# Kernel optimization log

Measured on AMD Instinct MI355X. Metric: run time of the kernel, lower is better.

Reference implementation:

```python
import jax, jax.numpy as jnp
import numpy as np

K = 20  # number of nearest neighbors (includes self, distance 0, as in torch topk(largest=False))


def edge_feature(x, k):
    """x: (B, C, N) -> edge features (B, N, k, 2C) = concat[central, neighbor - central]."""
    sq = jnp.sum(x * x, axis=1)                       # (B, N)
    inner = jnp.einsum('bcn,bcm->bnm', x, x)          # (B, N, N)
    d = sq[:, :, None] + sq[:, None, :] - 2.0 * inner # squared pairwise distance
    _, idx = jax.lax.top_k(-d, k)                     # (B, N, k) nearest indices (incl. self)
    xT = jnp.transpose(x, (0, 2, 1))                  # (B, N, C)
    # nb[b,n,j,c] = xT[b, idx[b,n,j], c]
    nb = jnp.take_along_axis(xT[:, :, None, :], idx[:, :, :, None], axis=1)  # (B, N, k, C)
    central = jnp.broadcast_to(xT[:, :, None, :], nb.shape)
    return jnp.concatenate([central, nb - central], axis=-1)  # (B, N, k, 2C)


def setup_inputs() -> dict:
    key = jax.random.key(0)
    ks = jax.random.split(key, 13)
    B, C, N = 8, 3, 4096
    def w(k_, shape, fan_in):
        return (jax.random.normal(k_, shape, dtype=jnp.float32) / np.sqrt(fan_in)).astype(jnp.float32)
    inp = {
        'x':  jax.random.normal(ks[0], (B, C, N), dtype=jnp.float32),
        # local 1x1 conv2d weights (out_ch, in_ch)
        'W1': w(ks[1], (64, 6), 6),        'b1': jnp.zeros((64,), jnp.float32),
        'W2': w(ks[2], (128, 64), 64),     'b2': jnp.zeros((128,), jnp.float32),
        # inter 1x1 conv1d
        'W3': w(ks[3], (1024, 128), 128),  'b3': jnp.zeros((1024,), jnp.float32),
        # global FC
        'W4': w(ks[4], (512, 1024), 1024), 'b4': jnp.zeros((512,), jnp.float32),
        'W5': w(ks[5], (256, 512), 512),   'b5': jnp.zeros((256,), jnp.float32),
        # final linear (torch inits this to zeros -> identity output; use small random for a
        # non-trivial correctness baseline, same math path)
        'W6': 0.01 * w(ks[6], (9, 256), 256), 'b6': jnp.zeros((9,), jnp.float32),
    }
    return inp


def reference(x, W1, b1, W2, b2, W3, b3, W4, b4, W5, b5, W6, b6):
    e = edge_feature(x, K)                                     # (B, N, k, 6)
    h = jax.nn.relu(jnp.einsum('bnkc,oc->bnko', e, W1) + b1)   # (B, N, k, 64)
    h = jax.nn.relu(jnp.einsum('bnkc,oc->bnko', h, W2) + b2)   # (B, N, k, 128)
    h = jnp.max(h, axis=2)                                     # max over k -> (B, N, 128)
    h = jax.nn.relu(jnp.einsum('bnc,oc->bno', h, W3) + b3)     # (B, N, 1024)
    g = jnp.max(h, axis=1)                                     # max over points -> (B, 1024)
    g = jax.nn.relu(g @ W4.T + b4)                             # (B, 512)
    g = jax.nn.relu(g @ W5.T + b5)                             # (B, 256)
    t = g @ W6.T + b6                                          # (B, 9)
    Bsz = x.shape[0]
    out_ch, in_ch = 3, 3
    t = t.reshape(Bsz, out_ch, in_ch) + jnp.eye(out_ch, in_ch, dtype=t.dtype)
    return t
```

## Files before the change

kernel.cpp:

```cpp
#include <hip/hip_runtime.h>
#include <hip/hip_bf16.h>
#include <cstdint>

#define B_SZ 8
#define NPTS 4096
#define KNN  20
#define NTOT (B_SZ * NPTS)
#define PPB  8
#define NPREP 1093

typedef unsigned int uint;
typedef unsigned short ushort;
using short8 = __attribute__((ext_vector_type(8))) short;
using f32x4  = __attribute__((ext_vector_type(4))) float;

__device__ __forceinline__ ushort f2bf(float f) {
  uint u = __float_as_uint(f);
  u += 0x7fff + ((u >> 16) & 1);
  return (ushort)(u >> 16);
}
__device__ __forceinline__ float bf2f(ushort h) {
  return __uint_as_float(((uint)h) << 16);
}
__device__ __forceinline__ uint fenc(float f) {
  uint u = __float_as_uint(f);
  return (u & 0x80000000u) ? ~u : (u | 0x80000000u);
}
__device__ __forceinline__ float fdec(uint e) {
  uint u = (e & 0x80000000u) ? (e & 0x7fffffffu) : ~e;
  return __uint_as_float(u);
}

__device__ __forceinline__ void sortf64(float& v, int lane) {
  #pragma unroll
  for (int k = 2; k <= 64; k <<= 1) {
    #pragma unroll
    for (int j = k >> 1; j > 0; j >>= 1) {
      float o = __shfl_xor(v, j, 64);
      bool keepmin = (((lane & k) == 0) == ((lane & j) == 0));
      bool lt = v < o;
      v = (keepmin == lt) ? v : o;
    }
  }
}

__device__ __forceinline__ void sortu64(unsigned long long& v, int lane) {
  #pragma unroll
  for (int k = 2; k <= 64; k <<= 1) {
    #pragma unroll
    for (int j = k >> 1; j > 0; j >>= 1) {
      unsigned long long o = __shfl_xor(v, j, 64);
      bool keepmin = (((lane & k) == 0) == ((lane & j) == 0));
      bool lt = v < o;
      v = (keepmin == lt) ? v : o;
    }
  }
}

__global__ void knn_prep_kernel(
    const float* __restrict__ x,  const float* __restrict__ W1,
    const float* __restrict__ W3, const float* __restrict__ W2,
    ushort* __restrict__ u, ushort* __restrict__ W3b, ushort* __restrict__ W2b,
    uint* __restrict__ g_enc, int* __restrict__ idx_out) {
  __shared__ int surv[4][256];
  __shared__ int cnt[4];

  if (blockIdx.x < NPREP) {
    int blk = blockIdx.x;
    if (blk < 1024) {
      int t = blk * 256 + threadIdx.x;
      int p = t >> 3, c0 = (t & 7) * 8;
      int b = p >> 12, n = p & (NPTS - 1);
      const float* xb = x + (size_t)b * 3 * NPTS;
      float x0 = xb[n], x1 = xb[NPTS + n], x2 = xb[2 * NPTS + n];
      uint pk[4];
      #pragma unroll
      for (int j = 0; j < 8; ++j) {
        const float* w = W1 + (c0 + j) * 6;
        float v = w[3] * x0 + w[4] * x1 + w[5] * x2;
        ushort h = f2bf(v);
        if (j & 1) pk[j >> 1] |= ((uint)h << 16); else pk[j >> 1] = h;
      }
      uint4 q; q.x = pk[0]; q.y = pk[1]; q.z = pk[2]; q.w = pk[3];
      *reinterpret_cast<uint4*>(u + (size_t)p * 64 + c0) = q;
    } else if (blk < 1088) {
      int t = (blk - 1024) * 256 + threadIdx.x;
      const float4* src = reinterpret_cast<const float4*>(W3 + t * 8);
      float4 f0 = src[0], f1 = src[1];
      uint4 pk;
      pk.x = (uint)f2bf(f0.x) | ((uint)f2bf(f0.y) << 16);
      pk.y = (uint)f2bf(f0.z) | ((uint)f2bf(f0.w) << 16);
      pk.z = (uint)f2bf(f1.x) | ((uint)f2bf(f1.y) << 16);
      pk.w = (uint)f2bf(f1.z) | ((uint)f2bf(f1.w) << 16);
      *reinterpret_cast<uint4*>(W3b + t * 8) = pk;
    } else if (blk < 1092) {
      int t = (blk - 1088) * 256 + threadIdx.x;
      const float4* src = reinterpret_cast<const float4*>(W2 + t * 8);
      float4 f0 = src[0], f1 = src[1];
      uint4 pk;
      pk.x = (uint)f2bf(f0.x) | ((uint)f2bf(f0.y) << 16);
      pk.y = (uint)f2bf(f0.z) | ((uint)f2bf(f0.w) << 16);
      pk.z = (uint)f2bf(f1.x) | ((uint)f2bf(f1.y) << 16);
      pk.w = (uint)f2bf(f1.z) | ((uint)f2bf(f1.w) << 16);
      *reinterpret_cast<uint4*>(W2b + t * 8) = pk;
    } else {
      for (int i = threadIdx.x; i < B_SZ * 1024; i += 256) g_enc[i] = 0;
    }
    return;
  }

  const unsigned long long INFK = ~0ull;
  int w = threadIdx.x >> 6, lane = threadIdx.x & 63;
  int row = (blockIdx.x - NPREP) * 4 + w;
  int b = row >> 12, n = row & (NPTS - 1);
  const float* xb = x + (size_t)b * 3 * NPTS;
  float qx = xb[n], qy = xb[NPTS + n], qz = xb[2 * NPTS + n];
  if (lane == 0) cnt[w] = 0;

  const float4* X0 = reinterpret_cast<const float4*>(xb);
  const float4* X1 = reinterpret_cast<const float4*>(xb + NPTS);
  const float4* X2 = reinterpret_cast<const float4*>(xb + 2 * NPTS);

  uint kreg[32];
  float bm = 3.0e38f;
  #pragma unroll
  for (int i = 0; i < 16; ++i) {
    int v4 = i * 64 + lane;
    float4 a0 = X0[v4], a1 = X1[v4], a2 = X2[v4];
    float dx, dy, dz, d0, d1, d2, d3;
    dx = a0.x - qx; dy = a1.x - qy; dz = a2.x - qz; d0 = dx*dx + dy*dy + dz*dz;
    dx = a0.y - qx; dy = a1.y - qy; dz = a2.y - qz; d1 = dx*dx + dy*dy + dz*dz;
    dx = a0.z - qx; dy = a1.z - qy; dz = a2.z - qz; d2 = dx*dx + dy*dy + dz*dz;
    dx = a0.w - qx; dy = a1.w - qy; dz = a2.w - qz; d3 = dx*dx + dy*dy + dz*dz;
    bm = fminf(bm, fminf(fminf(d0, d1), fminf(d2, d3)));
    kreg[2*i]   = (__float_as_uint(d0) >> 16) | (__float_as_uint(d1) & 0xFFFF0000u);
    kreg[2*i+1] = (__float_as_uint(d2) >> 16) | (__float_as_uint(d3) & 0xFFFF0000u);
  }

  sortf64(bm, lane);
  float T = __shfl(bm, 19, 64);
  uint T16 = __float_as_uint(T) >> 16;

  asm volatile("s_waitcnt lgkmcnt(0)" ::: "memory");
  #pragma unroll
  for (int i = 0; i < 16; ++i) {
    uint ka = kreg[2*i], kb = kreg[2*i+1];
    int m0 = (i * 64 + lane) * 4;
    if ((ka & 0xffffu) <= T16) { int s = atomicAdd(&cnt[w], 1); if (s < 256) surv[w][s] = m0; }
    if ((ka >> 16)     <= T16) { int s = atomicAdd(&cnt[w], 1); if (s < 256) surv[w][s] = m0 + 1; }
    if ((kb & 0xffffu) <= T16) { int s = atomicAdd(&cnt[w], 1); if (s < 256) surv[w][s] = m0 + 2; }
    if ((kb >> 16)     <= T16) { int s = atomicAdd(&cnt[w], 1); if (s < 256) surv[w][s] = m0 + 3; }
  }
  asm volatile("s_waitcnt lgkmcnt(0)" ::: "memory");
  int M = cnt[w];

  if (M <= 256) {
    unsigned long long run = INFK;
    int nch = (M + 63) >> 6;
    for (int c = 0; c < nch; ++c) {
      int s = c * 64 + lane;
      unsigned long long v = INFK;
      if (s < M) {
        int m = surv[w][s];
        float dx = xb[m] - qx, dy = xb[NPTS + m] - qy, dz = xb[2 * NPTS + m] - qz;
        float d = dx * dx + dy * dy + dz * dz;
        v = ((unsigned long long)__float_as_uint(d) << 32) | (unsigned)m;
      }
      sortu64(v, lane);
      if (c == 0) {
        run = v;
      } else {
        unsigned long long b19 = __shfl(v, (19 - lane) & 63, 64);
        unsigned long long cand = run < b19 ? run : b19;
        run = (lane < KNN) ? cand : INFK;
        sortu64(run, lane);
      }
    }
    if (lane < KNN) idx_out[(size_t)row * KNN + lane] = (int)(run & 0xFFFFFFFFull);
  } else {
    unsigned long long prev = 0ull;
    for (int r = 0; r < KNN; ++r) {
      unsigned long long best = INFK;
      for (int i = 0; i < 16; ++i) {
        int v4 = i * 64 + lane;
        float4 a0 = X0[v4], a1 = X1[v4], a2 = X2[v4];
        float dx, dy, dz, d[4];
        dx = a0.x - qx; dy = a1.x - qy; dz = a2.x - qz; d[0] = dx*dx + dy*dy + dz*dz;
        dx = a0.y - qx; dy = a1.y - qy; dz = a2.y - qz; d[1] = dx*dx + dy*dy + dz*dz;
        dx = a0.z - qx; dy = a1.z - qy; dz = a2.z - qz; d[2] = dx*dx + dy*dy + dz*dz;
        dx = a0.w - qx; dy = a1.w - qy; dz = a2.w - qz; d[3] = dx*dx + dy*dy + dz*dz;
        #pragma unroll
        for (int j = 0; j < 4; ++j) {
          int m = i * 256 + lane * 4 + j;
          unsigned long long key =
              ((unsigned long long)__float_as_uint(d[j]) << 32) | (unsigned)m;
          if ((r == 0 || key > prev) && key < best) best = key;
        }
      }
      #pragma unroll
      for (int off = 32; off; off >>= 1) {
        unsigned long long o = __shfl_xor(best, off, 64);
        best = o < best ? o : best;
      }
      if (lane == 0) idx_out[(size_t)row * KNN + r] = (int)(best & 0xFFFFFFFFull);
      prev = best;
    }
  }
}

__global__ __launch_bounds__(256, 4) void edge_kernel(
    const float* __restrict__ x,  const float* __restrict__ W1, const float* __restrict__ b1,
    const ushort* __restrict__ W2b, const float* __restrict__ b2,
    const ushort* __restrict__ u, const int* __restrict__ idx,
    ushort* __restrict__ h128b) {
  __shared__ __align__(16) char h1s[PPB * 32 * 128];
  __shared__ float vs[PPB * 64];
  __shared__ int   nbs[PPB * KNN];

  int tid = threadIdx.x, w = tid >> 6, l = tid & 63;
  int p0 = blockIdx.x * PPB;
  int b = p0 >> 12;
  const float* xb = x + (size_t)b * 3 * NPTS;

  for (int t = tid; t < PPB * 64; t += 256) {
    int p = t >> 6, c = t & 63;
    int n = (p0 + p) & (NPTS - 1);
    float x0 = xb[n], x1 = xb[NPTS + n], x2 = xb[2 * NPTS + n];
    const float* wr = W1 + c * 6;
    vs[t] = (wr[0] - wr[3]) * x0 + (wr[1] - wr[4]) * x1 + (wr[2] - wr[5]) * x2 + b1[c];
  }
  if (tid < PPB * KNN) nbs[tid] = idx[(size_t)p0 * KNN + tid];

  short8 bfr[8][2];
  #pragma unroll
  for (int nt = 0; nt < 8; ++nt) {
    #pragma unroll
    for (int ks = 0; ks < 2; ++ks) {
      bfr[nt][ks] = *(const short8*)(W2b + (nt * 16 + (l & 15)) * 64
                                         + ks * 32 + (l >> 4) * 8);
    }
  }
  __syncthreads();

  const ushort* ub = u + (((size_t)b) << 12) * 64;
  #pragma unroll
  for (int j = 0; j < 8; ++j) {
    int e_loc = j * 8 + (l >> 3);
    int p_loc = (w << 1) + (e_loc >> 5);
    int e_in = e_loc & 31;
    int e_src = (e_in < KNN) ? e_in : e_in - KNN;
    int nb = nbs[p_loc * KNN + e_src];
    int c0 = (l & 7) * 8;
    uint4 uv = *(const uint4*)(ub + (((size_t)nb) << 6) + c0);
    const float* vp = vs + p_loc * 64 + c0;
    float4 v0 = *(const float4*)vp, v1 = *(const float4*)(vp + 4);
    float h0 = fmaxf(bf2f((ushort)(uv.x & 0xffff)) + v0.x, 0.f);
    float h1 = fmaxf(bf2f((ushort)(uv.x >> 16))    + v0.y, 0.f);
    float h2 = fmaxf(bf2f((ushort)(uv.y & 0xffff)) + v0.z, 0.f);
    float h3 = fmaxf(bf2f((ushort)(uv.y >> 16))    + v0.w, 0.f);
    float h4 = fmaxf(bf2f((ushort)(uv.z & 0xffff)) + v1.x, 0.f);
    float h5 = fmaxf(bf2f((ushort)(uv.z >> 16))    + v1.y, 0.f);
    float h6 = fmaxf(bf2f((ushort)(uv.w & 0xffff)) + v1.z, 0.f);
    float h7 = fmaxf(bf2f((ushort)(uv.w >> 16))    + v1.w, 0.f);
    uint4 pk;
    pk.x = (uint)f2bf(h0) | ((uint)f2bf(h1) << 16);
    pk.y = (uint)f2bf(h2) | ((uint)f2bf(h3) << 16);
    pk.z = (uint)f2bf(h4) | ((uint)f2bf(h5) << 16);
    pk.w = (uint)f2bf(h6) | ((uint)f2bf(h7) << 16);
    int row = (w << 6) + e_loc;
    int byte = (row * 128 + c0 * 2) ^ ((row & 7) << 4);
    *(uint4*)(h1s + byte) = pk;
  }
  __syncthreads();

  float bias0 = b2[l], bias1 = b2[64 + l];

  #pragma unroll
  for (int pt = 0; pt < 2; ++pt) {
    int rbase = (w << 6) + (pt << 5);
    short8 a[2][2];
    #pragma unroll
    for (int m = 0; m < 2; ++m) {
      #pragma unroll
      for (int ks = 0; ks < 2; ++ks) {
        int row = rbase + m * 16 + (l & 15);
        int byte = (row * 128 + ks * 64 + (l >> 4) * 16) ^ ((row & 7) << 4);
        a[m][ks] = *(const short8*)(h1s + byte);
      }
    }
    float r03 = 0.f, r47 = 0.f;
    #pragma unroll
    for (int nt = 0; nt < 8; ++nt) {
      f32x4 acc0 = {0.f, 0.f, 0.f, 0.f}, acc1 = {0.f, 0.f, 0.f, 0.f};
      acc0 = __builtin_amdgcn_mfma_f32_16x16x32_bf16(a[0][0], bfr[nt][0], acc0, 0, 0, 0);
      acc0 = __builtin_amdgcn_mfma_f32_16x16x32_bf16(a[0][1], bfr[nt][1], acc0, 0, 0, 0);
      acc1 = __builtin_amdgcn_mfma_f32_16x16x32_bf16(a[1][0], bfr[nt][0], acc1, 0, 0, 0);
      acc1 = __builtin_amdgcn_mfma_f32_16x16x32_bf16(a[1][1], bfr[nt][1], acc1, 0, 0, 0);
      float m0 = fmaxf(fmaxf(fmaxf(acc0[0], acc1[0]), fmaxf(acc0[1], acc1[1])),
                       fmaxf(fmaxf(acc0[2], acc1[2]), fmaxf(acc0[3], acc1[3])));
      m0 = fmaxf(m0, __shfl_xor(m0, 16, 64));
      m0 = fmaxf(m0, __shfl_xor(m0, 32, 64));
      if ((l >> 4) == (nt & 3)) { if (nt < 4) r03 = m0; else r47 = m0; }
    }
    int pg = p0 + (w << 1) + pt;
    h128b[(size_t)pg * 128 + l]      = f2bf(fmaxf(r03 + bias0, 0.f));
    h128b[(size_t)pg * 128 + 64 + l] = f2bf(fmaxf(r47 + bias1, 0.f));
  }
}

__global__ __launch_bounds__(256, 2) void inter_kernel(
    const ushort* __restrict__ h128b, const ushort* __restrict__ W3b,
    uint* __restrict__ g_enc) {
  __shared__ __align__(16) char as_[64 * 256];
  int tid = threadIdx.x, w = tid >> 6, l = tid & 63;
  int chunk = blockIdx.x;
  const ushort* hp = h128b + (size_t)chunk * 64 * 128;

  {
    int row = tid >> 2, q = tid & 3;
    const uint4* src = reinterpret_cast<const uint4*>(hp + row * 128 + q * 32);
    int sw = (row & 7) << 4;
    int base = row * 256 + q * 64;
    #pragma unroll
    for (int k = 0; k < 4; ++k)
      *(uint4*)(as_ + ((base + k * 16) ^ sw)) = src[k];
  }
  __syncthreads();

  short8 a[4][4];
  #pragma unroll
  for (int m = 0; m < 4; ++m) {
    #pragma unroll
    for (int ks = 0; ks < 4; ++ks) {
      int row = m * 16 + (l & 15);
      int byte = (row * 256 + ks * 64 + (l >> 4) * 16) ^ ((row & 7) << 4);
      a[m][ks] = *(const short8*)(as_ + byte);
    }
  }

  const ushort* wb = W3b + (size_t)(w * 256) * 128;
  float res[4];
  #pragma unroll
  for (int nt = 0; nt < 16; ++nt) {
    f32x4 acc0 = {0.f,0.f,0.f,0.f}, acc1 = {0.f,0.f,0.f,0.f};
    f32x4 acc2 = {0.f,0.f,0.f,0.f}, acc3 = {0.f,0.f,0.f,0.f};
    #pragma unroll
    for (int ks = 0; ks < 4; ++ks) {
      short8 bf = *(const short8*)(wb + (size_t)(nt * 16 + (l & 15)) * 128
                                      + ks * 32 + (l >> 4) * 8);
      acc0 = __builtin_amdgcn_mfma_f32_16x16x32_bf16(a[0][ks], bf, acc0, 0, 0, 0);
      acc1 = __builtin_amdgcn_mfma_f32_16x16x32_bf16(a[1][ks], bf, acc1, 0, 0, 0);
      acc2 = __builtin_amdgcn_mfma_f32_16x16x32_bf16(a[2][ks], bf, acc2, 0, 0, 0);
      acc3 = __builtin_amdgcn_mfma_f32_16x16x32_bf16(a[3][ks], bf, acc3, 0, 0, 0);
    }
    float m01 = fmaxf(fmaxf(fmaxf(acc0[0], acc1[0]), fmaxf(acc0[1], acc1[1])),
                      fmaxf(fmaxf(acc0[2], acc1[2]), fmaxf(acc0[3], acc1[3])));
    float m23 = fmaxf(fmaxf(fmaxf(acc2[0], acc3[0]), fmaxf(acc2[1], acc3[1])),
                      fmaxf(fmaxf(acc2[2], acc3[2]), fmaxf(acc2[3], acc3[3])));
    float m0 = fmaxf(m01, m23);
    m0 = fmaxf(m0, __shfl_xor(m0, 16, 64));
    m0 = fmaxf(m0, __shfl_xor(m0, 32, 64));
    if ((l >> 4) == (nt & 3)) res[nt >> 2] = m0;
  }
  uint* ge = g_enc + (size_t)(chunk >> 6) * 1024 + w * 256;
  #pragma unroll
  for (int g = 0; g < 4; ++g) atomicMax(ge + g * 64 + l, fenc(res[g]));
}

__global__ __launch_bounds__(64) void fc_kernel(const float* __restrict__ in,
                                                const uint* __restrict__ enc,
                                                const float* __restrict__ pre_b,
                                                const float* __restrict__ W,
                                                const float* __restrict__ bias,
                                                float* __restrict__ out,
                                                int in_dim, int out_dim, int mode) {
  int blk = blockIdx.x;
  int b = blk / out_dim, o = blk % out_dim;
  int lane = threadIdx.x;
  const float* w = W + (size_t)o * in_dim;
  float s = 0.f;
  for (int c = lane; c < in_dim; c += 64) {
    float v;
    if (mode == 2) v = fmaxf(fdec(enc[(size_t)b * in_dim + c]) + pre_b[c], 0.f);
    else           v = in[(size_t)b * in_dim + c];
    s += v * w[c];
  }
  #pragma unroll
  for (int off = 32; off; off >>= 1) s += __shfl_down(s, off);
  if (lane == 0) {
    float r = s + bias[o];
    if (mode != 1) r = fmaxf(r, 0.0f);
    else if (o == 0 || o == 4 || o == 8) r += 1.0f;
    out[blk] = r;
  }
}

extern "C" void kernel_launch(void* const* d_in, const int* in_sizes, int n_in,
                              void* d_out, int out_size, void* d_ws, size_t ws_size,
                              hipStream_t stream) {
  const float* x  = (const float*)d_in[0];
  const float* W1 = (const float*)d_in[1];
  const float* b1 = (const float*)d_in[2];
  const float* W2 = (const float*)d_in[3];
  const float* b2 = (const float*)d_in[4];
  const float* W3 = (const float*)d_in[5];
  const float* b3 = (const float*)d_in[6];
  const float* W4 = (const float*)d_in[7];
  const float* b4 = (const float*)d_in[8];
  const float* W5 = (const float*)d_in[9];
  const float* b5 = (const float*)d_in[10];
  const float* W6 = (const float*)d_in[11];
  const float* b6 = (const float*)d_in[12];
  float* out = (float*)d_out;

  char* ws = (char*)d_ws;
  ushort* u_bf  = (ushort*)(ws);
  int*    idxb  = (int*)  (ws + (8u  << 20));
  ushort* h128b = (ushort*)(ws + (11u << 20));
  ushort* W3b   = (ushort*)(ws + (27u << 20));
  ushort* W2b   = (ushort*)(ws + (27u << 20) + (256u << 10));
  uint*   g_enc = (uint*) (ws + (5u  << 20));
  float*  g4    = (float*)(ws + (6u  << 20));
  float*  g5    = (float*)(ws + (7u  << 20));

  hipLaunchKernelGGL(knn_prep_kernel, dim3(NPREP + 8192), dim3(256), 0, stream,
                     x, W1, W3, W2, u_bf, W3b, W2b, g_enc, idxb);
  hipLaunchKernelGGL(edge_kernel, dim3(NTOT / PPB), dim3(256), 0, stream,
                     x, W1, b1, W2b, b2, u_bf, idxb, h128b);
  hipLaunchKernelGGL(inter_kernel, dim3(512), dim3(256), 0, stream, h128b, W3b, g_enc);
  hipLaunchKernelGGL(fc_kernel, dim3(B_SZ * 512), dim3(64), 0, stream,
                     nullptr, g_enc, b3, W4, b4, g4, 1024, 512, 2);
  hipLaunchKernelGGL(fc_kernel, dim3(B_SZ * 256), dim3(64), 0, stream,
                     g4, nullptr, nullptr, W5, b5, g5, 512, 256, 0);
  hipLaunchKernelGGL(fc_kernel, dim3(B_SZ * 9),   dim3(64), 0, stream,
                     g5, nullptr, nullptr, W6, b6, out, 256, 9, 1);
}
```

Before: 167.6 us.

## Process two KNN query rows per wavefront to share point loads and interleave sorts

Each wavefront now handles two query points instead of one. The float4 loads of the point cloud are shared between both distance computations, and the bitonic shuffle sorts are run on two values at once to expose instruction-level parallelism. The KNN portion of the grid is halved to match. This cuts redundant global/L2 loads and shuffle latency stalls, at the cost of roughly doubled register use (two 32-entry key arrays) and possibly lower occupancy.

```diff
diff --git a/kernel.cpp b/kernel.cpp
--- a/kernel.cpp
+++ b/kernel.cpp
@@ -31,28 +31,31 @@
   return __uint_as_float(u);
 }
 
-__device__ __forceinline__ void sortf64(float& v, int lane) {
+__device__ __forceinline__ void sortf64x2(float& v0, float& v1, int lane) {
   #pragma unroll
   for (int k = 2; k <= 64; k <<= 1) {
     #pragma unroll
     for (int j = k >> 1; j > 0; j >>= 1) {
-      float o = __shfl_xor(v, j, 64);
+      float o0 = __shfl_xor(v0, j, 64);
+      float o1 = __shfl_xor(v1, j, 64);
       bool keepmin = (((lane & k) == 0) == ((lane & j) == 0));
-      bool lt = v < o;
-      v = (keepmin == lt) ? v : o;
-    }
-  }
-}
-
-__device__ __forceinline__ void sortu64(unsigned long long& v, int lane) {
+      bool lt0 = v0 < o0; v0 = (keepmin == lt0) ? v0 : o0;
+      bool lt1 = v1 < o1; v1 = (keepmin == lt1) ? v1 : o1;
+    }
+  }
+}
+
+__device__ __forceinline__ void sortu64x2(unsigned long long& v0,
+                                          unsigned long long& v1, int lane) {
   #pragma unroll
   for (int k = 2; k <= 64; k <<= 1) {
     #pragma unroll
     for (int j = k >> 1; j > 0; j >>= 1) {
-      unsigned long long o = __shfl_xor(v, j, 64);
+      unsigned long long o0 = __shfl_xor(v0, j, 64);
+      unsigned long long o1 = __shfl_xor(v1, j, 64);
       bool keepmin = (((lane & k) == 0) == ((lane & j) == 0));
-      bool lt = v < o;
-      v = (keepmin == lt) ? v : o;
+      bool lt0 = v0 < o0; v0 = (keepmin == lt0) ? v0 : o0;
+      bool lt1 = v1 < o1; v1 = (keepmin == lt1) ? v1 : o1;
     }
   }
 }
@@ -62,8 +65,8 @@
     const float* __restrict__ W3, const float* __restrict__ W2,
     ushort* __restrict__ u, ushort* __restrict__ W3b, ushort* __restrict__ W2b,
     uint* __restrict__ g_enc, int* __restrict__ idx_out) {
-  __shared__ int surv[4][256];
-  __shared__ int cnt[4];
+  __shared__ int surv[8][256];
+  __shared__ int cnt[8];
 
   if (blockIdx.x < NPREP) {
     int blk = blockIdx.x;
@@ -111,73 +114,107 @@
 
   const unsigned long long INFK = ~0ull;
   int w = threadIdx.x >> 6, lane = threadIdx.x & 63;
-  int row = (blockIdx.x - NPREP) * 4 + w;
-  int b = row >> 12, n = row & (NPTS - 1);
+  int row0 = ((blockIdx.x - NPREP) * 4 + w) * 2;
+  int b = row0 >> 12;
+  int n0 = row0 & (NPTS - 1), n1 = n0 + 1;
   const float* xb = x + (size_t)b * 3 * NPTS;
-  float qx = xb[n], qy = xb[NPTS + n], qz = xb[2 * NPTS + n];
-  if (lane == 0) cnt[w] = 0;
+  float q0x = xb[n0], q0y = xb[NPTS + n0], q0z = xb[2 * NPTS + n0];
+  float q1x = xb[n1], q1y = xb[NPTS + n1], q1z = xb[2 * NPTS + n1];
+  if (lane == 0) { cnt[2 * w] = 0; cnt[2 * w + 1] = 0; }
 
   const float4* X0 = reinterpret_cast<const float4*>(xb);
   const float4* X1 = reinterpret_cast<const float4*>(xb + NPTS);
   const float4* X2 = reinterpret_cast<const float4*>(xb + 2 * NPTS);
 
-  uint kreg[32];
-  float bm = 3.0e38f;
+  uint kregA[32], kregB[32];
+  float bm0 = 3.0e38f, bm1 = 3.0e38f;
   #pragma unroll
   for (int i = 0; i < 16; ++i) {
     int v4 = i * 64 + lane;
     float4 a0 = X0[v4], a1 = X1[v4], a2 = X2[v4];
     float dx, dy, dz, d0, d1, d2, d3;
-    dx = a0.x - qx; dy = a1.x - qy; dz = a2.x - qz; d0 = dx*dx + dy*dy + dz*dz;
-    dx = a0.y - qx; dy = a1.y - qy; dz = a2.y - qz; d1 = dx*dx + dy*dy + dz*dz;
-    dx = a0.z - qx; dy = a1.z - qy; dz = a2.z - qz; d2 = dx*dx + dy*dy + dz*dz;
-    dx = a0.w - qx; dy = a1.w - qy; dz = a2.w - qz; d3 = dx*dx + dy*dy + dz*dz;
-    bm = fminf(bm, fminf(fminf(d0, d1), fminf(d2, d3)));
-    kreg[2*i]   = (__float_as_uint(d0) >> 16) | (__float_as_uint(d1) & 0xFFFF0000u);
-    kreg[2*i+1] = (__float_as_uint(d2) >> 16) | (__float_as_uint(d3) & 0xFFFF0000u);
-  }
-
-  sortf64(bm, lane);
-  float T = __shfl(bm, 19, 64);
-  uint T16 = __float_as_uint(T) >> 16;
+    dx = a0.x - q0x; dy = a1.x - q0y; dz = a2.x - q0z; d0 = dx*dx + dy*dy + dz*dz;
+    dx = a0.y - q0x; dy = a1.y - q0y; dz = a2.y - q0z; d1 = dx*dx + dy*dy + dz*dz;
+    dx = a0.z - q0x; dy = a1.z - q0y; dz = a2.z - q0z; d2 = dx*dx + dy*dy + dz*dz;
+    dx = a0.w - q0x; dy = a1.w - q0y; dz = a2.w - q0z; d3 = dx*dx + dy*dy + dz*dz;
+    bm0 = fminf(bm0, fminf(fminf(d0, d1), fminf(d2, d3)));
+    kregA[2*i]   = (__float_as_uint(d0) >> 16) | (__float_as_uint(d1) & 0xFFFF0000u);
+    kregA[2*i+1] = (__float_as_uint(d2) >> 16) | (__float_as_uint(d3) & 0xFFFF0000u);
+    dx = a0.x - q1x; dy = a1.x - q1y; dz = a2.x - q1z; d0 = dx*dx + dy*dy + dz*dz;
+    dx = a0.y - q1x; dy = a1.y - q1y; dz = a2.y - q1z; d1 = dx*dx + dy*dy + dz*dz;
+    dx = a0.z - q1x; dy = a1.z - q1y; dz = a2.z - q1z; d2 = dx*dx + dy*dy + dz*dz;
+    dx = a0.w - q1x; dy = a1.w - q1y; dz = a2.w - q1z; d3 = dx*dx + dy*dy + dz*dz;
+    bm1 = fminf(bm1, fminf(fminf(d0, d1), fminf(d2, d3)));
+    kregB[2*i]   = (__float_as_uint(d0) >> 16) | (__float_as_uint(d1) & 0xFFFF0000u);
+    kregB[2*i+1] = (__float_as_uint(d2) >> 16) | (__float_as_uint(d3) & 0xFFFF0000u);
+  }
+
+  sortf64x2(bm0, bm1, lane);
+  float T0 = __shfl(bm0, 19, 64), T1 = __shfl(bm1, 19, 64);
+  uint T016 = __float_as_uint(T0) >> 16, T116 = __float_as_uint(T1) >> 16;
 
   asm volatile("s_waitcnt lgkmcnt(0)" ::: "memory");
   #pragma unroll
   for (int i = 0; i < 16; ++i) {
-    uint ka = kreg[2*i], kb = kreg[2*i+1];
     int m0 = (i * 64 + lane) * 4;
-    if ((ka & 0xffffu) <= T16) { int s = atomicAdd(&cnt[w], 1); if (s < 256) surv[w][s] = m0; }
-    if ((ka >> 16)     <= T16) { int s = atomicAdd(&cnt[w], 1); if (s < 256) surv[w][s] = m0 + 1; }
-    if ((kb & 0xffffu) <= T16) { int s = atomicAdd(&cnt[w], 1); if (s < 256) surv[w][s] = m0 + 2; }
-    if ((kb >> 16)     <= T16) { int s = atomicAdd(&cnt[w], 1); if (s < 256) surv[w][s] = m0 + 3; }
+    uint ka = kregA[2*i], kb = kregA[2*i+1];
+    if ((ka & 0xffffu) <= T016) { int s = atomicAdd(&cnt[2*w], 1); if (s < 256) surv[2*w][s] = m0; }
+    if ((ka >> 16)     <= T016) { int s = atomicAdd(&cnt[2*w], 1); if (s < 256) surv[2*w][s] = m0 + 1; }
+    if ((kb & 0xffffu) <= T016) { int s = atomicAdd(&cnt[2*w], 1); if (s < 256) surv[2*w][s] = m0 + 2; }
+    if ((kb >> 16)     <= T016) { int s = atomicAdd(&cnt[2*w], 1); if (s < 256) surv[2*w][s] = m0 + 3; }
+    uint kc = kregB[2*i], kd = kregB[2*i+1];
+    if ((kc & 0xffffu) <= T116) { int s = atomicAdd(&cnt[2*w+1], 1); if (s < 256) surv[2*w+1][s] = m0; }
+    if ((kc >> 16)     <= T116) { int s = atomicAdd(&cnt[2*w+1], 1); if (s < 256) surv[2*w+1][s] = m0 + 1; }
+    if ((kd & 0xffffu) <= T116) { int s = atomicAdd(&cnt[2*w+1], 1); if (s < 256) surv[2*w+1][s] = m0 + 2; }
+    if ((kd >> 16)     <= T116) { int s = atomicAdd(&cnt[2*w+1], 1); if (s < 256) surv[2*w+1][s] = m0 + 3; }
   }
   asm volatile("s_waitcnt lgkmcnt(0)" ::: "memory");
-  int M = cnt[w];
-
-  if (M <= 256) {
-    unsigned long long run = INFK;
-    int nch = (M + 63) >> 6;
+  int M0 = cnt[2*w], M1 = cnt[2*w+1];
+
+  {
+    int M0c = M0 <= 256 ? M0 : 0, M1c = M1 <= 256 ? M1 : 0;
+    int nch = ((M0c > M1c ? M0c : M1c) + 63) >> 6;
+    unsigned long long run0 = INFK, run1 = INFK;
     for (int c = 0; c < nch; ++c) {
       int s = c * 64 + lane;
-      unsigned long long v = INFK;
-      if (s < M) {
-        int m = surv[w][s];
-        float dx = xb[m] - qx, dy = xb[NPTS + m] - qy, dz = xb[2 * NPTS + m] - qz;
+      unsigned long long v0 = INFK, v1 = INFK;
+      if (s < M0c) {
+        int m = surv[2*w][s];
+        float dx = xb[m] - q0x, dy = xb[NPTS + m] - q0y, dz = xb[2 * NPTS + m] - q0z;
         float d = dx * dx + dy * dy + dz * dz;
-        v = ((unsigned long long)__float_as_uint(d) << 32) | (unsigned)m;
-      }
-      sortu64(v, lane);
+        v0 = ((unsigned long long)__float_as_uint(d) << 32) | (unsigned)m;
+      }
+      if (s < M1c) {
+        int m = surv[2*w+1][s];
+        float dx = xb[m] - q1x, dy = xb[NPTS + m] - q1y, dz = xb[2 * NPTS + m] - q1z;
+        float d = dx * dx + dy * dy + dz * dz;
+        v1 = ((unsigned long long)__float_as_uint(d) << 32) | (unsigned)m;
+      }
+      sortu64x2(v0, v1, lane);
       if (c == 0) {
-        run = v;
+        run0 = v0; run1 = v1;
       } else {
-        unsigned long long b19 = __shfl(v, (19 - lane) & 63, 64);
-        unsigned long long cand = run < b19 ? run : b19;
-        run = (lane < KNN) ? cand : INFK;
-        sortu64(run, lane);
-      }
-    }
-    if (lane < KNN) idx_out[(size_t)row * KNN + lane] = (int)(run & 0xFFFFFFFFull);
-  } else {
+        unsigned long long b0 = __shfl(v0, (19 - lane) & 63, 64);
+        unsigned long long b1 = __shfl(v1, (19 - lane) & 63, 64);
+        unsigned long long c0 = run0 < b0 ? run0 : b0;
+        unsigned long long c1 = run1 < b1 ? run1 : b1;
+        run0 = (lane < KNN) ? c0 : INFK;
+        run1 = (lane < KNN) ? c1 : INFK;
+        sortu64x2(run0, run1, lane);
+      }
+    }
+    if (M0 <= 256 && lane < KNN)
+      idx_out[(size_t)row0 * KNN + lane] = (int)(run0 & 0xFFFFFFFFull);
+    if (M1 <= 256 && lane < KNN)
+      idx_out[(size_t)(row0 + 1) * KNN + lane] = (int)(run1 & 0xFFFFFFFFull);
+  }
+
+  #pragma unroll 1
+  for (int rr = 0; rr < 2; ++rr) {
+    int M = rr ? M1 : M0;
+    if (M <= 256) continue;
+    float qx = rr ? q1x : q0x, qy = rr ? q1y : q0y, qz = rr ? q1z : q0z;
+    int row = row0 + rr;
     unsigned long long prev = 0ull;
     for (int r = 0; r < KNN; ++r) {
       unsigned long long best = INFK;
@@ -423,7 +460,7 @@
   float*  g4    = (float*)(ws + (6u  << 20));
   float*  g5    = (float*)(ws + (7u  << 20));
 
-  hipLaunchKernelGGL(knn_prep_kernel, dim3(NPREP + 8192), dim3(256), 0, stream,
+  hipLaunchKernelGGL(knn_prep_kernel, dim3(NPREP + 4096), dim3(256), 0, stream,
                      x, W1, W3, W2, u_bf, W3b, W2b, g_enc, idxb);
   hipLaunchKernelGGL(edge_kernel, dim3(NTOT / PPB), dim3(256), 0, stream,
                      x, W1, b1, W2b, b2, u_bf, idxb, h128b);
```

After: 197.1 us. 17.6% more time.
